# Kernel optimization log

Measured on AMD Instinct MI355X. Metric: run time of the kernel, lower is better.

The kernel has to match this reference:

```python
import jax, jax.numpy as jnp
import numpy as np

S = 4  # per-node signal width (hardcoded in the torch source)

def setup_inputs() -> dict:
    key = jax.random.key(0)
    ks = jax.random.split(key, 7)
    B, W, L = 32, 4096, 96
    sc = 0.3  # keep pre-sigmoid activations in a reasonable range
    return {
        "x": jax.random.uniform(ks[0], (B, W), dtype=jnp.float32),
        "w_top": jax.random.normal(ks[1], (W, 2 * S, S), dtype=jnp.float32) * sc,
        "b_top": jax.random.normal(ks[2], (W, 2 * S), dtype=jnp.float32) * sc,
        "w_gate": jax.random.normal(ks[3], (L, W, 2 * S, 2 * S), dtype=jnp.float32) * sc,
        "b_gate": jax.random.normal(ks[4], (L, W, 2 * S), dtype=jnp.float32) * sc,
        "w_prior": jax.random.normal(ks[5], (W, 1, 2 * S), dtype=jnp.float32) * sc,
        "b_prior": jax.random.normal(ks[6], (W, 1), dtype=jnp.float32) * sc,
    }

def _and_layer(xin, w, b):
    # AndNode: reshape -> Linear -> Sigmoid -> reshape (B, W, S, 2)
    # xin: [B, W, P*S]; w: [W, 2S, P*S]; b: [W, 2S]
    y = jax.nn.sigmoid(jnp.einsum('bwk,wok->bwo', xin, w) + b)
    Bn, Wn = y.shape[0], y.shape[1]
    # torch reshape (batch, 2S) -> (batch, S, 2): out[..., s, slot] = y[..., 2*s + slot]
    return y.reshape(Bn, Wn, S, 2)

def _route(out):
    # Parent j sends out-slot0 to child j and out-slot1 to child (j+1) % W.
    # Heap pops parents in DESCENDING rv order, so for child k>0 the concat slot
    # order is [out1 from parent k, out2 from parent k-1]; for child 0 parent W-1
    # is processed first: [out2 from parent W-1, out1 from parent 0].
    out1, out2 = out[..., 0], out[..., 1]                      # [B, W, S]
    slot0 = jnp.concatenate([out2[:, -1:], out1[:, 1:]], axis=1)
    slot1 = jnp.concatenate([out1[:, :1], out2[:, :-1]], axis=1)
    x = jnp.stack([slot0, slot1], axis=-1)                     # [B, W, S, 2]
    # torch reshape (batch, S, P) -> (batch, P*S): flatten in (s, p) order
    return x.reshape(x.shape[0], x.shape[1], 2 * S)

def reference(x, w_top, b_top, w_gate, b_gate, w_prior, b_prior):
    Bn, Wn = x.shape
    # Observed AND nodes (num_parents=1): input = observed bit replicated to S slots
    xin = jnp.broadcast_to(x[:, :, None], (Bn, Wn, S))
    h = _route(_and_layer(xin, w_top, b_top))
    def step(h, wb):
        w, b = wb
        return _route(_and_layer(h, w, b)), None
    h, _ = jax.lax.scan(step, h, (w_gate, b_gate))
    # PRIOR nodes: Linear(2S -> 1), NO sigmoid; output concatenated in rv order
    logits = jnp.einsum('bwk,wok->bwo', h, w_prior) + b_prior  # [B, W, 1]
    return logits[:, :, 0]
```

## Files before the change

kernel.cpp:

```cpp
#include <hip/hip_runtime.h>
#include <stdint.h>

#define WN 4096
#define BN 32
#define LN 96
#define CN 16
#define HN 16
#define NS (CN + HN)
#define NBLK (WN / CN)
#define TPB (NS * BN)
#define NSS (LN / HN)

#define POISON64 0xAAAAAAAAAAAAAAAAULL

#define RING_SS_STRIDE ((size_t)NBLK * CN * BN * 4)
#define RING2_OFF ((size_t)(NSS - 1) * RING_SS_STRIDE)

static __device__ __forceinline__ float sigmoid_f(float z) {
    float e = __builtin_amdgcn_exp2f(z * -1.4426950408889634f);
    return __builtin_amdgcn_rcpf(1.0f + e);
}

static __device__ __forceinline__ uint64_t pack2(float a, float b) {
    union { float f[2]; uint64_t u; } u;
    u.f[0] = a; u.f[1] = b;
    return u.u;
}

static __device__ __forceinline__ void unpack2(uint64_t q, float& a, float& b) {
    union { uint64_t u; float f[2]; } u;
    u.u = q; a = u.f[0]; b = u.f[1];
}

static __device__ __forceinline__ uint64_t poll64(const uint64_t* p) {
    uint64_t q;
    do {
        q = __hip_atomic_load(p, __ATOMIC_RELAXED, __HIP_MEMORY_SCOPE_AGENT);
    } while (q == POISON64 || q == 0ULL);
    return q;
}

__global__
__attribute__((amdgpu_flat_work_group_size(TPB, TPB), amdgpu_waves_per_eu(4, 4)))
void rh_halo_kernel(
    const float* __restrict__ x,
    const float* __restrict__ w_top,
    const float* __restrict__ b_top,
    const float* __restrict__ w_gate,
    const float* __restrict__ b_gate,
    const float* __restrict__ w_prior,
    const float* __restrict__ b_prior,
    float* __restrict__ out,
    uint64_t* __restrict__ ring)
{
    const int tid  = threadIdx.x;
    const int j    = tid >> 5;
    const int b    = tid & 31;
    const int blk  = blockIdx.x;
    const int node = (blk * CN - HN + j + WN) & (WN - 1);
    const bool isn0 = (node == 0);
    const int leftblk = (blk + NBLK - 1) & (NBLK - 1);

    __shared__ float4 lodds[2][NS][BN];

    float y[8];

    {
        float xv = x[(size_t)b * WN + node];
        const float4* wt = (const float4*)(w_top + (size_t)node * 32);
        const float4* bt = (const float4*)(b_top + (size_t)node * 8);
        float4 c0 = bt[0], c1 = bt[1];
        float bb[8] = {c0.x, c0.y, c0.z, c0.w, c1.x, c1.y, c1.z, c1.w};
        #pragma unroll
        for (int o = 0; o < 8; ++o) {
            float4 a = wt[o];
            y[o] = sigmoid_f(xv * (a.x + a.y + a.z + a.w) + bb[o]);
        }
    }

    const float4* wg_base = (const float4*)w_gate;
    const float4* bg_base = (const float4*)b_gate;
    int par = 0;

    #pragma unroll 1
    for (int ss = 0; ss < NSS; ++ss) {
        #pragma unroll 1
        for (int t = 1; t <= HN; ++t) {
            const int g = ss * HN + t;

            if (j >= t - 1)
                lodds[par][j][b] = make_float4(y[1], y[3], y[5], y[7]);

            __syncthreads();

            if (j >= t) {
                float4 od = lodds[par][j - 1][b];
                float h0, h1, h2, h3, h4, h5, h6, h7;
                if (isn0) {
                    h0 = od.x; h2 = od.y; h4 = od.z; h6 = od.w;
                    h1 = y[0]; h3 = y[2]; h5 = y[4]; h7 = y[6];
                } else {
                    h0 = y[0]; h2 = y[2]; h4 = y[4]; h6 = y[6];
                    h1 = od.x; h3 = od.y; h5 = od.z; h7 = od.w;
                }
                const float4* wrow = wg_base + ((size_t)(g - 1) * WN + node) * 16;
                const float4* brow = bg_base + ((size_t)(g - 1) * WN + node) * 2;
                float4 c0 = brow[0], c1 = brow[1];
                float z[8] = {c0.x, c0.y, c0.z, c0.w, c1.x, c1.y, c1.z, c1.w};
                #pragma unroll
                for (int o = 0; o < 8; ++o) {
                    float4 a0 = wrow[2 * o], a1 = wrow[2 * o + 1];
                    z[o] += a0.x * h0 + a0.y * h1 + a0.z * h2 + a0.w * h3
                          + a1.x * h4 + a1.y * h5 + a1.z * h6 + a1.w * h7;
                }
                #pragma unroll
                for (int o = 0; o < 8; ++o) y[o] = sigmoid_f(z[o]);
            }
            par ^= 1;
        }

        if (ss < NSS - 1) {
            if (j >= HN) {
                uint64_t* slot = ring + (size_t)ss * RING_SS_STRIDE
                               + (((size_t)blk * CN + (j - HN)) * BN + b) * 4;
                __hip_atomic_store(slot + 0, pack2(y[0], y[1]),
                                   __ATOMIC_RELAXED, __HIP_MEMORY_SCOPE_AGENT);
                __hip_atomic_store(slot + 1, pack2(y[2], y[3]),
                                   __ATOMIC_RELAXED, __HIP_MEMORY_SCOPE_AGENT);
                __hip_atomic_store(slot + 2, pack2(y[4], y[5]),
                                   __ATOMIC_RELAXED, __HIP_MEMORY_SCOPE_AGENT);
                __hip_atomic_store(slot + 3, pack2(y[6], y[7]),
                                   __ATOMIC_RELAXED, __HIP_MEMORY_SCOPE_AGENT);
            } else {
                const uint64_t* src = ring + (size_t)ss * RING_SS_STRIDE
                                    + (((size_t)leftblk * CN + j) * BN + b) * 4;
                unpack2(poll64(src + 0), y[0], y[1]);
                unpack2(poll64(src + 1), y[2], y[3]);
                unpack2(poll64(src + 2), y[4], y[5]);
                unpack2(poll64(src + 3), y[6], y[7]);
            }
        }
    }

    if (j >= HN)
        lodds[par][j][b] = make_float4(y[1], y[3], y[5], y[7]);
    if (j == NS - 1) {
        uint64_t* slot = ring + RING2_OFF + ((size_t)blk * BN + b) * 2;
        __hip_atomic_store(slot + 0, pack2(y[1], y[3]),
                           __ATOMIC_RELAXED, __HIP_MEMORY_SCOPE_AGENT);
        __hip_atomic_store(slot + 1, pack2(y[5], y[7]),
                           __ATOMIC_RELAXED, __HIP_MEMORY_SCOPE_AGENT);
    }
    __syncthreads();

    if (j >= HN) {
        float od0, od1, od2, od3;
        if (j == HN) {
            const uint64_t* src = ring + RING2_OFF + ((size_t)leftblk * BN + b) * 2;
            unpack2(poll64(src + 0), od0, od1);
            unpack2(poll64(src + 1), od2, od3);
        } else {
            float4 t = lodds[par][j - 1][b];
            od0 = t.x; od1 = t.y; od2 = t.z; od3 = t.w;
        }
        float h0, h1, h2, h3, h4, h5, h6, h7;
        if (isn0) {
            h0 = od0;  h2 = od1;  h4 = od2;  h6 = od3;
            h1 = y[0]; h3 = y[2]; h5 = y[4]; h7 = y[6];
        } else {
            h0 = y[0]; h2 = y[2]; h4 = y[4]; h6 = y[6];
            h1 = od0;  h3 = od1;  h5 = od2;  h7 = od3;
        }
        const float4* wp = (const float4*)(w_prior + (size_t)node * 8);
        float4 p0 = wp[0], p1 = wp[1];
        float logit = b_prior[node]
            + p0.x * h0 + p0.y * h1 + p0.z * h2 + p0.w * h3
            + p1.x * h4 + p1.y * h5 + p1.z * h6 + p1.w * h7;
        out[(size_t)b * WN + node] = logit;
    }
}

extern "C" void kernel_launch(void* const* d_in, const int* in_sizes, int n_in,
                              void* d_out, int out_size, void* d_ws, size_t ws_size,
                              hipStream_t stream) {
    const float* x       = (const float*)d_in[0];
    const float* w_top   = (const float*)d_in[1];
    const float* b_top   = (const float*)d_in[2];
    const float* w_gate  = (const float*)d_in[3];
    const float* b_gate  = (const float*)d_in[4];
    const float* w_prior = (const float*)d_in[5];
    const float* b_prior = (const float*)d_in[6];
    float* out           = (float*)d_out;
    uint64_t* ring       = (uint64_t*)d_ws;

    hipLaunchKernelGGL(rh_halo_kernel, dim3(NBLK), dim3(TPB), 0, stream,
                       x, w_top, b_top, w_gate, b_gate, w_prior, b_prior,
                       out, ring);
}
```

Before: 383.4 us.

## Give each thread four batch rows and prefetch next-layer gate weights into registers

Each thread now handles four batch elements instead of one, so a block is 256 threads instead of 1024. The per-node gate weights are loaded once per layer and reused across the four batch rows rather than reloaded by 32 threads. The next layer's weights are prefetched into registers during the current step to hide global load latency. The cost is fewer threads to hide latency, more register pressure (waves_per_eu set to 1), and more serial work per thread on the dependency chain.

```diff
diff --git a/kernel.cpp b/kernel.cpp
--- a/kernel.cpp
+++ b/kernel.cpp
@@ -7,8 +7,9 @@
 #define CN 16
 #define HN 16
 #define NS (CN + HN)
+#define GQ 8
+#define TPB (NS * GQ)
 #define NBLK (WN / CN)
-#define TPB (NS * BN)
 #define NSS (LN / HN)
 
 #define POISON64 0xAAAAAAAAAAAAAAAAULL
@@ -41,8 +42,8 @@
 }
 
 __global__
-__attribute__((amdgpu_flat_work_group_size(TPB, TPB), amdgpu_waves_per_eu(4, 4)))
-void rh_halo_kernel(
+__attribute__((amdgpu_flat_work_group_size(TPB, TPB), amdgpu_waves_per_eu(1, 1)))
+void rh_halo_g4_kernel(
     const float* __restrict__ x,
     const float* __restrict__ w_top,
     const float* __restrict__ b_top,
@@ -54,8 +55,8 @@
     uint64_t* __restrict__ ring)
 {
     const int tid  = threadIdx.x;
-    const int j    = tid >> 5;
-    const int b    = tid & 31;
+    const int j    = tid >> 3;
+    const int q    = tid & 7;
     const int blk  = blockIdx.x;
     const int node = (blk * CN - HN + j + WN) & (WN - 1);
     const bool isn0 = (node == 0);
@@ -63,120 +64,174 @@
 
     __shared__ float4 lodds[2][NS][BN];
 
-    float y[8];
+    float y[8][4];
 
     {
-        float xv = x[(size_t)b * WN + node];
         const float4* wt = (const float4*)(w_top + (size_t)node * 32);
         const float4* bt = (const float4*)(b_top + (size_t)node * 8);
         float4 c0 = bt[0], c1 = bt[1];
         float bb[8] = {c0.x, c0.y, c0.z, c0.w, c1.x, c1.y, c1.z, c1.w};
-        #pragma unroll
-        for (int o = 0; o < 8; ++o) {
-            float4 a = wt[o];
-            y[o] = sigmoid_f(xv * (a.x + a.y + a.z + a.w) + bb[o]);
+        float rs[8];
+        #pragma unroll
+        for (int o = 0; o < 8; ++o) { float4 a = wt[o]; rs[o] = a.x + a.y + a.z + a.w; }
+        #pragma unroll
+        for (int i = 0; i < 4; ++i) {
+            float xv = x[(size_t)(q * 4 + i) * WN + node];
+            #pragma unroll
+            for (int o = 0; o < 8; ++o) y[o][i] = sigmoid_f(xv * rs[o] + bb[o]);
         }
     }
 
     const float4* wg_base = (const float4*)w_gate;
     const float4* bg_base = (const float4*)b_gate;
+
+    float4 wa[16], wbl, wbh;
+    if (j >= 1) {
+        const float4* wrow = wg_base + (size_t)node * 16;
+        const float4* brow = bg_base + (size_t)node * 2;
+        #pragma unroll
+        for (int k = 0; k < 16; ++k) wa[k] = wrow[k];
+        wbl = brow[0]; wbh = brow[1];
+    }
+
     int par = 0;
 
     #pragma unroll 1
     for (int ss = 0; ss < NSS; ++ss) {
         #pragma unroll 1
         for (int t = 1; t <= HN; ++t) {
-            const int g = ss * HN + t;
-
-            if (j >= t - 1)
-                lodds[par][j][b] = make_float4(y[1], y[3], y[5], y[7]);
+            if (j >= t - 1) {
+                #pragma unroll
+                for (int m = 0; m < 4; ++m)
+                    lodds[par][j][m * 8 + q] =
+                        make_float4(y[2*m+1][0], y[2*m+1][1], y[2*m+1][2], y[2*m+1][3]);
+            }
 
             __syncthreads();
 
             if (j >= t) {
-                float4 od = lodds[par][j - 1][b];
-                float h0, h1, h2, h3, h4, h5, h6, h7;
-                if (isn0) {
-                    h0 = od.x; h2 = od.y; h4 = od.z; h6 = od.w;
-                    h1 = y[0]; h3 = y[2]; h5 = y[4]; h7 = y[6];
-                } else {
-                    h0 = y[0]; h2 = y[2]; h4 = y[4]; h6 = y[6];
-                    h1 = od.x; h3 = od.y; h5 = od.z; h7 = od.w;
-                }
-                const float4* wrow = wg_base + ((size_t)(g - 1) * WN + node) * 16;
-                const float4* brow = bg_base + ((size_t)(g - 1) * WN + node) * 2;
-                float4 c0 = brow[0], c1 = brow[1];
-                float z[8] = {c0.x, c0.y, c0.z, c0.w, c1.x, c1.y, c1.z, c1.w};
+                float h[8][4];
+                #pragma unroll
+                for (int m = 0; m < 4; ++m) {
+                    float4 od = lodds[par][j - 1][m * 8 + q];
+                    float odv[4] = {od.x, od.y, od.z, od.w};
+                    #pragma unroll
+                    for (int i = 0; i < 4; ++i) {
+                        h[2*m][i]   = isn0 ? odv[i]    : y[2*m][i];
+                        h[2*m+1][i] = isn0 ? y[2*m][i] : odv[i];
+                    }
+                }
+                float bb[8] = {wbl.x, wbl.y, wbl.z, wbl.w, wbh.x, wbh.y, wbh.z, wbh.w};
                 #pragma unroll
                 for (int o = 0; o < 8; ++o) {
-                    float4 a0 = wrow[2 * o], a1 = wrow[2 * o + 1];
-                    z[o] += a0.x * h0 + a0.y * h1 + a0.z * h2 + a0.w * h3
-                          + a1.x * h4 + a1.y * h5 + a1.z * h6 + a1.w * h7;
-                }
-                #pragma unroll
-                for (int o = 0; o < 8; ++o) y[o] = sigmoid_f(z[o]);
-            }
+                    float4 a0 = wa[2*o], a1 = wa[2*o+1];
+                    #pragma unroll
+                    for (int i = 0; i < 4; ++i) {
+                        float z = bb[o]
+                            + a0.x*h[0][i] + a0.y*h[1][i] + a0.z*h[2][i] + a0.w*h[3][i]
+                            + a1.x*h[4][i] + a1.y*h[5][i] + a1.z*h[6][i] + a1.w*h[7][i];
+                        y[o][i] = sigmoid_f(z);
+                    }
+                }
+            }
+
+            const int nlay = ss * HN + t;
+            const int tn = (t == HN) ? 1 : t + 1;
+            if (nlay < LN && j >= tn) {
+                const float4* wrow = wg_base + ((size_t)nlay * WN + node) * 16;
+                const float4* brow = bg_base + ((size_t)nlay * WN + node) * 2;
+                #pragma unroll
+                for (int k = 0; k < 16; ++k) wa[k] = wrow[k];
+                wbl = brow[0]; wbh = brow[1];
+            }
+
             par ^= 1;
         }
 
         if (ss < NSS - 1) {
             if (j >= HN) {
-                uint64_t* slot = ring + (size_t)ss * RING_SS_STRIDE
-                               + (((size_t)blk * CN + (j - HN)) * BN + b) * 4;
-                __hip_atomic_store(slot + 0, pack2(y[0], y[1]),
-                                   __ATOMIC_RELAXED, __HIP_MEMORY_SCOPE_AGENT);
-                __hip_atomic_store(slot + 1, pack2(y[2], y[3]),
-                                   __ATOMIC_RELAXED, __HIP_MEMORY_SCOPE_AGENT);
-                __hip_atomic_store(slot + 2, pack2(y[4], y[5]),
-                                   __ATOMIC_RELAXED, __HIP_MEMORY_SCOPE_AGENT);
-                __hip_atomic_store(slot + 3, pack2(y[6], y[7]),
-                                   __ATOMIC_RELAXED, __HIP_MEMORY_SCOPE_AGENT);
+                const int own = j - HN;
+                #pragma unroll
+                for (int i = 0; i < 4; ++i) {
+                    const int b = q * 4 + i;
+                    uint64_t* slot = ring + (size_t)ss * RING_SS_STRIDE
+                                   + (((size_t)blk * CN + own) * BN + b) * 4;
+                    __hip_atomic_store(slot + 0, pack2(y[0][i], y[1][i]),
+                                       __ATOMIC_RELAXED, __HIP_MEMORY_SCOPE_AGENT);
+                    __hip_atomic_store(slot + 1, pack2(y[2][i], y[3][i]),
+                                       __ATOMIC_RELAXED, __HIP_MEMORY_SCOPE_AGENT);
+                    __hip_atomic_store(slot + 2, pack2(y[4][i], y[5][i]),
+                                       __ATOMIC_RELAXED, __HIP_MEMORY_SCOPE_AGENT);
+                    __hip_atomic_store(slot + 3, pack2(y[6][i], y[7][i]),
+                                       __ATOMIC_RELAXED, __HIP_MEMORY_SCOPE_AGENT);
+                }
             } else {
-                const uint64_t* src = ring + (size_t)ss * RING_SS_STRIDE
-                                    + (((size_t)leftblk * CN + j) * BN + b) * 4;
-                unpack2(poll64(src + 0), y[0], y[1]);
-                unpack2(poll64(src + 1), y[2], y[3]);
-                unpack2(poll64(src + 2), y[4], y[5]);
-                unpack2(poll64(src + 3), y[6], y[7]);
-            }
-        }
-    }
-
-    if (j >= HN)
-        lodds[par][j][b] = make_float4(y[1], y[3], y[5], y[7]);
+                #pragma unroll
+                for (int i = 0; i < 4; ++i) {
+                    const int b = q * 4 + i;
+                    const uint64_t* src = ring + (size_t)ss * RING_SS_STRIDE
+                                        + (((size_t)leftblk * CN + j) * BN + b) * 4;
+                    unpack2(poll64(src + 0), y[0][i], y[1][i]);
+                    unpack2(poll64(src + 1), y[2][i], y[3][i]);
+                    unpack2(poll64(src + 2), y[4][i], y[5][i]);
+                    unpack2(poll64(src + 3), y[6][i], y[7][i]);
+                }
+            }
+        }
+    }
+
+    if (j >= HN) {
+        #pragma unroll
+        for (int m = 0; m < 4; ++m)
+            lodds[par][j][m * 8 + q] =
+                make_float4(y[2*m+1][0], y[2*m+1][1], y[2*m+1][2], y[2*m+1][3]);
+    }
     if (j == NS - 1) {
-        uint64_t* slot = ring + RING2_OFF + ((size_t)blk * BN + b) * 2;
-        __hip_atomic_store(slot + 0, pack2(y[1], y[3]),
-                           __ATOMIC_RELAXED, __HIP_MEMORY_SCOPE_AGENT);
-        __hip_atomic_store(slot + 1, pack2(y[5], y[7]),
-                           __ATOMIC_RELAXED, __HIP_MEMORY_SCOPE_AGENT);
+        #pragma unroll
+        for (int i = 0; i < 4; ++i) {
+            const int b = q * 4 + i;
+            uint64_t* slot = ring + RING2_OFF + ((size_t)blk * BN + b) * 2;
+            __hip_atomic_store(slot + 0, pack2(y[1][i], y[3][i]),
+                               __ATOMIC_RELAXED, __HIP_MEMORY_SCOPE_AGENT);
+            __hip_atomic_store(slot + 1, pack2(y[5][i], y[7][i]),
+                               __ATOMIC_RELAXED, __HIP_MEMORY_SCOPE_AGENT);
+        }
     }
     __syncthreads();
 
     if (j >= HN) {
-        float od0, od1, od2, od3;
+        float od[4][4];
         if (j == HN) {
-            const uint64_t* src = ring + RING2_OFF + ((size_t)leftblk * BN + b) * 2;
-            unpack2(poll64(src + 0), od0, od1);
-            unpack2(poll64(src + 1), od2, od3);
+            #pragma unroll
+            for (int i = 0; i < 4; ++i) {
+                const int b = q * 4 + i;
+                const uint64_t* src = ring + RING2_OFF + ((size_t)leftblk * BN + b) * 2;
+                unpack2(poll64(src + 0), od[0][i], od[1][i]);
+                unpack2(poll64(src + 1), od[2][i], od[3][i]);
+            }
         } else {
-            float4 t = lodds[par][j - 1][b];
-            od0 = t.x; od1 = t.y; od2 = t.z; od3 = t.w;
-        }
-        float h0, h1, h2, h3, h4, h5, h6, h7;
-        if (isn0) {
-            h0 = od0;  h2 = od1;  h4 = od2;  h6 = od3;
-            h1 = y[0]; h3 = y[2]; h5 = y[4]; h7 = y[6];
-        } else {
-            h0 = y[0]; h2 = y[2]; h4 = y[4]; h6 = y[6];
-            h1 = od0;  h3 = od1;  h5 = od2;  h7 = od3;
+            #pragma unroll
+            for (int m = 0; m < 4; ++m) {
+                float4 t4 = lodds[par][j - 1][m * 8 + q];
+                od[m][0] = t4.x; od[m][1] = t4.y; od[m][2] = t4.z; od[m][3] = t4.w;
+            }
         }
         const float4* wp = (const float4*)(w_prior + (size_t)node * 8);
         float4 p0 = wp[0], p1 = wp[1];
-        float logit = b_prior[node]
-            + p0.x * h0 + p0.y * h1 + p0.z * h2 + p0.w * h3
-            + p1.x * h4 + p1.y * h5 + p1.z * h6 + p1.w * h7;
-        out[(size_t)b * WN + node] = logit;
+        float bp = b_prior[node];
+        #pragma unroll
+        for (int i = 0; i < 4; ++i) {
+            float h[8];
+            #pragma unroll
+            for (int m = 0; m < 4; ++m) {
+                h[2*m]   = isn0 ? od[m][i]  : y[2*m][i];
+                h[2*m+1] = isn0 ? y[2*m][i] : od[m][i];
+            }
+            float logit = bp
+                + p0.x*h[0] + p0.y*h[1] + p0.z*h[2] + p0.w*h[3]
+                + p1.x*h[4] + p1.y*h[5] + p1.z*h[6] + p1.w*h[7];
+            out[(size_t)(q * 4 + i) * WN + node] = logit;
+        }
     }
 }
 
@@ -193,7 +248,7 @@
     float* out           = (float*)d_out;
     uint64_t* ring       = (uint64_t*)d_ws;
 
-    hipLaunchKernelGGL(rh_halo_kernel, dim3(NBLK), dim3(TPB), 0, stream,
+    hipLaunchKernelGGL(rh_halo_g4_kernel, dim3(NBLK), dim3(TPB), 0, stream,
                        x, w_top, b_top, w_gate, b_gate, w_prior, b_prior,
                        out, ring);
 }
```

Measured after the change: 341.4 us. -11.0%, faster.
